# Kernel optimization log

Hardware: AMD Instinct MI355X
Metric: run time of the kernel (lower is better)

The kernel has to match this reference:

```python
import jax, jax.numpy as jnp
import numpy as np
import math

N, S, D, H, L, F = 4, 2048, 512, 8, 4, 200
HD = D // H
EPS = 1e-5


def _pos_encoding(seq_len, d_model, dtype):
    pos = jnp.arange(seq_len, dtype=jnp.float32)[:, None]            # [S,1]
    div = jnp.exp(jnp.arange(0, d_model, 2, dtype=jnp.float32) * (-math.log(10000.0) / d_model))
    ang = pos * div                                                   # [S,D/2]
    pe = jnp.stack([jnp.sin(ang), jnp.cos(ang)], axis=-1).reshape(seq_len, d_model)
    return pe.astype(dtype)


def _layernorm(x, w, b):
    mu = jnp.mean(x, axis=-1, keepdims=True)
    var = jnp.mean(jnp.square(x - mu), axis=-1, keepdims=True)
    return (x - mu) * jax.lax.rsqrt(var + EPS) * w + b


def setup_inputs() -> dict:
    key = jax.random.key(0)
    ks = jax.random.split(key, 8)
    std = 0.02
    inp = {
        "features": jax.random.normal(ks[0], (N, S, D), dtype=jnp.float32),
        # attention projections, stored as [L, in, out] (math-equivalent to torch x @ W.T + b)
        "Wq": jax.random.normal(ks[1], (L, D, D), dtype=jnp.float32) * std,
        "bq": jnp.zeros((L, D), dtype=jnp.float32),
        "Wk": jax.random.normal(ks[2], (L, D, D), dtype=jnp.float32) * std,
        "bk": jnp.zeros((L, D), dtype=jnp.float32),
        "Wv": jax.random.normal(ks[3], (L, D, D), dtype=jnp.float32) * std,
        "bv": jnp.zeros((L, D), dtype=jnp.float32),
        "Wo": jax.random.normal(ks[4], (L, D, D), dtype=jnp.float32) * std,
        "bo": jnp.zeros((L, D), dtype=jnp.float32),
        # FFN
        "W1": jax.random.normal(ks[5], (L, D, F), dtype=jnp.float32) * std,
        "b1": jnp.zeros((L, F), dtype=jnp.float32),
        "W2": jax.random.normal(ks[6], (L, F, D), dtype=jnp.float32) * std,
        "b2": jnp.zeros((L, D), dtype=jnp.float32),
        # layernorms
        "ln1_w": jnp.ones((L, D), dtype=jnp.float32),
        "ln1_b": jnp.zeros((L, D), dtype=jnp.float32),
        "ln2_w": jnp.ones((L, D), dtype=jnp.float32),
        "ln2_b": jnp.zeros((L, D), dtype=jnp.float32),
    }
    return inp


def _encoder(features, Wq, bq, Wk, bk, Wv, bv, Wo, bo, W1, b1, W2, b2,
             ln1_w, ln1_b, ln2_w, ln2_b):
    n, s, d = features.shape
    x = features + _pos_encoding(s, d, features.dtype)[None]  # PositionalEncoding (dropout=identity in eval)
    scale = 1.0 / math.sqrt(HD)
    for l in range(L):
        # MultiHeadAttention: manual QK^T -> softmax -> AV
        q = (x @ Wq[l] + bq[l]).reshape(n, s, H, HD)
        k = (x @ Wk[l] + bk[l]).reshape(n, s, H, HD)
        v = (x @ Wv[l] + bv[l]).reshape(n, s, H, HD)
        attn = jnp.einsum("nshd,nthd->nhst", q, k) * scale          # [N,H,S,S]
        score = jax.nn.softmax(attn, axis=-1)
        y = jnp.einsum("nhst,nthd->nshd", score, v).reshape(n, s, d)
        attn_out = y @ Wo[l] + bo[l]
        x = _layernorm(x + attn_out, ln1_w[l], ln1_b[l])
        # FFN: linear2(relu(linear1(x)))
        ff = jax.nn.relu(x @ W1[l] + b1[l]) @ W2[l] + b2[l]
        x = _layernorm(x + ff, ln2_w[l], ln2_b[l])
    return x


def reference(features, Wq, bq, Wk, bk, Wv, bv, Wo, bo, W1, b1, W2, b2,
              ln1_w, ln1_b, ln2_w, ln2_b):
    return _encoder(features, Wq, bq, Wk, bk, Wv, bv, Wo, bo, W1, b1, W2, b2,
                    ln1_w, ln1_b, ln2_w, ln2_b)
```

## Files before the change

### kernel.cpp

```cpp
#include <hip/hip_runtime.h>
#include <hip/hip_bf16.h>
#include <cstdint>


typedef __bf16 bf16;
typedef __bf16 bf16x8 __attribute__((ext_vector_type(8)));
typedef __bf16 bf16x4 __attribute__((ext_vector_type(4)));
typedef float f32x4 __attribute__((ext_vector_type(4)));

#define MFMA16(a, b, c) __builtin_amdgcn_mfma_f32_16x16x32_bf16((a), (b), (c), 0, 0, 0)

static constexpr int NB   = 4;
static constexpr int SQ   = 2048;
static constexpr int DM   = 512;
static constexpr int NH   = 8;
static constexpr int HD   = 64;
static constexpr int NL   = 4;
static constexpr int FF   = 200;
static constexpr int FFP  = 256;
static constexpr int MTOK = NB * SQ;

__device__ __forceinline__ float fast_exp2(float x) {
#if __has_builtin(__builtin_amdgcn_exp2f)
    return __builtin_amdgcn_exp2f(x);
#else
    return exp2f(x);
#endif
}

__device__ __forceinline__ void gld16(bf16* l, const bf16* g) {
    __builtin_amdgcn_global_load_lds(
        (const __attribute__((address_space(1))) void*)g,
        (__attribute__((address_space(3))) void*)l, 16, 0, 0);
}

__global__ __launch_bounds__(256) void convw_kernel(
    const float* __restrict__ Wq, const float* __restrict__ Wk,
    const float* __restrict__ Wv, const float* __restrict__ Wo,
    const float* __restrict__ W1, const float* __restrict__ W2,
    bf16* __restrict__ wqkvt, bf16* __restrict__ wot,
    bf16* __restrict__ w1t, bf16* __restrict__ w2t)
{
    __shared__ float tile[32][33];
    const int z = blockIdx.z, l = z / 6, which = z % 6;
    const float* src; bf16* dst; int K, Nsrc, Npad, Kpad;
    switch (which) {
        case 0: src = Wq + (size_t)l*DM*DM; dst = wqkvt + (size_t)(l*3+0)*DM*DM; K=DM; Nsrc=DM; Npad=DM; Kpad=DM; break;
        case 1: src = Wk + (size_t)l*DM*DM; dst = wqkvt + (size_t)(l*3+1)*DM*DM; K=DM; Nsrc=DM; Npad=DM; Kpad=DM; break;
        case 2: src = Wv + (size_t)l*DM*DM; dst = wqkvt + (size_t)(l*3+2)*DM*DM; K=DM; Nsrc=DM; Npad=DM; Kpad=DM; break;
        case 3: src = Wo + (size_t)l*DM*DM; dst = wot   + (size_t)l*DM*DM;       K=DM; Nsrc=DM; Npad=DM; Kpad=DM; break;
        case 4: src = W1 + (size_t)l*DM*FF; dst = w1t   + (size_t)l*FFP*DM;      K=DM; Nsrc=FF; Npad=FFP; Kpad=DM; break;
        default:src = W2 + (size_t)l*FF*DM; dst = w2t   + (size_t)l*DM*FFP;      K=FF; Nsrc=DM; Npad=DM; Kpad=FFP; break;
    }
    const int k0 = blockIdx.x * 32, n0 = blockIdx.y * 32;
    if (k0 >= Kpad || n0 >= Npad) return;
    const int tr = threadIdx.x >> 3, tc = (threadIdx.x & 7) * 4;
    for (int c = 0; c < 4; c++) {
        int sr = k0 + tr, sc = n0 + tc + c;
        tile[tr][tc + c] = (sr < K && sc < Nsrc) ? src[(size_t)sr * Nsrc + sc] : 0.f;
    }
    __syncthreads();
    const int dr = n0 + tr;
    if (dr < Npad) {
        for (int c = 0; c < 4; c++) {
            int dc = k0 + tc + c;
            if (dc < Kpad) dst[(size_t)dr * Kpad + dc] = (bf16)tile[tc + c][tr];
        }
    }
}

__global__ __launch_bounds__(256) void posenc_kernel(
    const float* __restrict__ f, float* __restrict__ x, bf16* __restrict__ xb)
{
    const int t = blockIdx.x * 256 + threadIdx.x;
    const int d2 = t & 255, row = t >> 8, s = row & (SQ - 1);
    const float kfac = -0.03597789207803197f;
    float dv = __expf((float)d2 * kfac);
    float ang = (float)s * dv;
    float pe0 = sinf(ang), pe1 = cosf(ang);
    const size_t base = (size_t)row * DM + d2 * 2;
    float2 fv = *(const float2*)(f + base);
    float o0 = fv.x + pe0, o1 = fv.y + pe1;
    *(float2*)(x + base) = make_float2(o0, o1);
    union { bf16 h[2]; unsigned int u; } pk;
    pk.h[0] = (bf16)o0; pk.h[1] = (bf16)o1;
    *(unsigned int*)(xb + base) = pk.u;
}

__device__ __forceinline__ void gemm128_core(
    const bf16* __restrict__ A, const bf16* __restrict__ Wt, int K,
    int m0, int n0, bf16* As, bf16* Bs, f32x4 (&acc)[4][4])
{
    const int tid = threadIdx.x;
    const int w = tid >> 6, lane = tid & 63;
    const int l15 = lane & 15, quad = lane >> 4;
    const int srow = w * 16 + (lane >> 2);
    const int scol = (lane & 3) * 8;
    const bf16* Ag = A  + (size_t)(m0 + srow) * K + scol;
    const bf16* Bg = Wt + (size_t)(n0 + srow) * K + scol;
    bf16* AsW = As + w * 512;
    bf16* BsW = Bs + w * 512;
    const int wm = (w >> 1) * 64, wn = (w & 1) * 64;

    for (int k0 = 0; k0 < K; k0 += 32) {
        __syncthreads();
        gld16(AsW,        Ag + k0);
        gld16(AsW + 2048, Ag + (size_t)64 * K + k0);
        gld16(BsW,        Bg + k0);
        gld16(BsW + 2048, Bg + (size_t)64 * K + k0);
        asm volatile("s_waitcnt vmcnt(0)" ::: "memory");
        __syncthreads();

        bf16x8 af[4], bfr[4];
        #pragma unroll
        for (int i = 0; i < 4; i++)
            af[i] = *(const bf16x8*)&As[(wm + i * 16 + l15) * 32 + quad * 8];
        #pragma unroll
        for (int j = 0; j < 4; j++)
            bfr[j] = *(const bf16x8*)&Bs[(wn + j * 16 + l15) * 32 + quad * 8];
        #pragma unroll
        for (int i = 0; i < 4; i++)
            #pragma unroll
            for (int j = 0; j < 4; j++)
                acc[i][j] = MFMA16(af[i], bfr[j], acc[i][j]);
    }
}

__global__ __launch_bounds__(256, 3) void gemm64_kernel(
    const bf16* __restrict__ A, const bf16* __restrict__ Wt,
    const float* __restrict__ bias, int nbias,
    float* __restrict__ outf, bf16* __restrict__ outb,
    int K, int Nc, int mode)
{
    __shared__ alignas(16) bf16 As[128 * 32];
    __shared__ alignas(16) bf16 Bs[64 * 32];
    const int m0 = blockIdx.x * 128, n0 = blockIdx.y * 64;
    const int tid = threadIdx.x;
    const int w = tid >> 6, lane = tid & 63;
    const int l15 = lane & 15, quad = lane >> 4;
    const int srow = w * 16 + (lane >> 2);
    const int scol = (lane & 3) * 8;
    const bf16* Ag = A  + (size_t)(m0 + srow) * K + scol;
    const bf16* Bg = Wt + (size_t)(n0 + srow) * K + scol;
    bf16* AsW = As + w * 512;
    bf16* BsW = Bs + w * 512;
    const int wm = (w >> 1) * 64, wn = (w & 1) * 32;
    f32x4 acc[4][2] = {};

    for (int k0 = 0; k0 < K; k0 += 32) {
        __syncthreads();
        gld16(AsW,        Ag + k0);
        gld16(AsW + 2048, Ag + (size_t)64 * K + k0);
        gld16(BsW,        Bg + k0);
        asm volatile("s_waitcnt vmcnt(0)" ::: "memory");
        __syncthreads();

        bf16x8 af[4], bfr[2];
        #pragma unroll
        for (int i = 0; i < 4; i++)
            af[i] = *(const bf16x8*)&As[(wm + i * 16 + l15) * 32 + quad * 8];
        #pragma unroll
        for (int j = 0; j < 2; j++)
            bfr[j] = *(const bf16x8*)&Bs[(wn + j * 16 + l15) * 32 + quad * 8];
        #pragma unroll
        for (int i = 0; i < 4; i++)
            #pragma unroll
            for (int j = 0; j < 2; j++)
                acc[i][j] = MFMA16(af[i], bfr[j], acc[i][j]);
    }

    #pragma unroll
    for (int j = 0; j < 2; j++) {
        const int col = n0 + wn + j * 16 + l15;
        const float bv = (col < nbias) ? bias[col] : 0.f;
        #pragma unroll
        for (int i = 0; i < 4; i++) {
            const int rbase = m0 + wm + i * 16 + quad * 4;
            #pragma unroll
            for (int r = 0; r < 4; r++) {
                float v = acc[i][j][r] + bv;
                const int row = rbase + r;
                const size_t idx = (size_t)row * Nc + col;
                if (mode == 0)      outf[idx] = v;
                else if (mode == 1) outb[idx] = (bf16)v;
                else                outb[idx] = (bf16)fmaxf(v, 0.f);
            }
        }
    }
}

__global__ __launch_bounds__(256, 3) void gemm_wo_kernel(
    const bf16* __restrict__ o0, const bf16* __restrict__ o1,
    const float* __restrict__ lpart,
    const bf16* __restrict__ Wt, const float* __restrict__ bias,
    float* __restrict__ outf)
{
    __shared__ alignas(16) bf16 As[128 * 32];
    __shared__ alignas(16) bf16 Bs[64 * 32];
    const int m0 = blockIdx.x * 128, n0 = blockIdx.y * 64;
    const int tid = threadIdx.x;
    const int w = tid >> 6, lane = tid & 63;
    const int l15 = lane & 15, quad = lane >> 4;
    const int srow = w * 16 + (lane >> 2);
    const int scol = (lane & 3) * 8;
    const int row0 = m0 + srow, row1 = row0 + 64;
    const bf16* Bg = Wt + (size_t)(n0 + srow) * DM + scol;
    bf16* BsW = Bs + w * 512;
    bf16* AsD0 = As + w * 512 + lane * 8;
    bf16* AsD1 = AsD0 + 2048;
    const int wm = (w >> 1) * 64, wn = (w & 1) * 32;

    const int b0 = (((row0 >> 11) * 8) << 11) | (row0 & (SQ - 1));
    const int b1 = (((row1 >> 11) * 8) << 11) | (row1 & (SQ - 1));
    float rl0[8], rl1[8];
    #pragma unroll
    for (int h = 0; h < 8; h++) {
        rl0[h] = 1.f / (lpart[b0 + (h << 11)] + lpart[65536 + b0 + (h << 11)]);
        rl1[h] = 1.f / (lpart[b1 + (h << 11)] + lpart[65536 + b1 + (h << 11)]);
    }

    const bf16* A0g  = o0 + (size_t)row0 * DM + scol;
    const bf16* A0g2 = o0 + (size_t)row1 * DM + scol;
    const bf16* A1g  = o1 + (size_t)row0 * DM + scol;
    const bf16* A1g2 = o1 + (size_t)row1 * DM + scol;
    f32x4 acc[4][2] = {};

    #pragma unroll
    for (int h = 0; h < 8; h++) {
        #pragma unroll
        for (int kk = 0; kk < 2; kk++) {
            const int k0 = h * 64 + kk * 32;
            __syncthreads();
            bf16x8 a0 = *(const bf16x8*)(A0g  + k0);
            bf16x8 c0 = *(const bf16x8*)(A1g  + k0);
            bf16x8 a1 = *(const bf16x8*)(A0g2 + k0);
            bf16x8 c1 = *(const bf16x8*)(A1g2 + k0);
            gld16(BsW, Bg + k0);
            bf16x8 s0, s1;
            #pragma unroll
            for (int i = 0; i < 8; i++) {
                s0[i] = (bf16)(((float)a0[i] + (float)c0[i]) * rl0[h]);
                s1[i] = (bf16)(((float)a1[i] + (float)c1[i]) * rl1[h]);
            }
            *(bf16x8*)AsD0 = s0;
            *(bf16x8*)AsD1 = s1;
            asm volatile("s_waitcnt vmcnt(0)" ::: "memory");
            __syncthreads();

            bf16x8 af[4], bfr[2];
            #pragma unroll
            for (int i = 0; i < 4; i++)
                af[i] = *(const bf16x8*)&As[(wm + i * 16 + l15) * 32 + quad * 8];
            #pragma unroll
            for (int j = 0; j < 2; j++)
                bfr[j] = *(const bf16x8*)&Bs[(wn + j * 16 + l15) * 32 + quad * 8];
            #pragma unroll
            for (int i = 0; i < 4; i++)
                #pragma unroll
                for (int j = 0; j < 2; j++)
                    acc[i][j] = MFMA16(af[i], bfr[j], acc[i][j]);
        }
    }

    #pragma unroll
    for (int j = 0; j < 2; j++) {
        const int col = n0 + wn + j * 16 + l15;
        const float bv = bias[col];
        #pragma unroll
        for (int i = 0; i < 4; i++) {
            const int rbase = m0 + wm + i * 16 + quad * 4;
            #pragma unroll
            for (int r = 0; r < 4; r++)
                outf[(size_t)(rbase + r) * DM + col] = acc[i][j][r] + bv;
        }
    }
}

__global__ __launch_bounds__(256, 3) void gemm128_qkv_kernel(
    const bf16* __restrict__ xb, const bf16* __restrict__ Wt,
    const float* __restrict__ bq, const float* __restrict__ bk,
    const float* __restrict__ bv,
    bf16* __restrict__ qb, bf16* __restrict__ kb, bf16* __restrict__ vtb)
{
    __shared__ alignas(16) bf16 As[128 * 32];
    __shared__ alignas(16) bf16 Bs[128 * 32];
    const int m0 = blockIdx.x * 128, n0 = blockIdx.y * 128;
    f32x4 acc[4][4] = {};
    gemm128_core(xb, Wt, DM, m0, n0, As, Bs, acc);

    const int lane = threadIdx.x & 63;
    const int l15 = lane & 15, quad = lane >> 4;
    const int w = threadIdx.x >> 6;
    const int wm = (w >> 1) * 64, wn = (w & 1) * 64;
    const int which = n0 >> 9;
    const float* bias = (which == 0) ? bq : (which == 1) ? bk : bv;
    const float scale = (which == 0) ? 0.18033688f : 1.f;
    #pragma unroll
    for (int j = 0; j < 4; j++) {
        const int c = (n0 & 511) + wn + j * 16 + l15;
        const float bvv = bias[c];
        #pragma unroll
        for (int i = 0; i < 4; i++) {
            const int rbase = m0 + wm + i * 16 + quad * 4;
            #pragma unroll
            for (int r = 0; r < 4; r++) {
                float v = (acc[i][j][r] + bvv) * scale;
                const int row = rbase + r;
                if (which == 0)      qb[(size_t)row * DM + c] = (bf16)v;
                else if (which == 1) kb[(size_t)row * DM + c] = (bf16)v;
                else {
                    const int n = row >> 11, s = row & (SQ - 1);
                    const int h = c >> 6, hd = c & 63;
                    vtb[((size_t)(((n << 3) | h) << 6 | hd) << 11) | s] = (bf16)v;
                }
            }
        }
    }
}

__global__ __launch_bounds__(256, 2) void attn_kernel(
    const bf16* __restrict__ qb, const bf16* __restrict__ kb,
    const bf16* __restrict__ vtb,
    bf16* __restrict__ opart0, bf16* __restrict__ opart1,
    float* __restrict__ lpart)
{
    __shared__ alignas(16) bf16 Kt[2][64][72];
    __shared__ alignas(16) bf16 Vt[2 * 64 * 68];
    const int tid = threadIdx.x;
    const int w = tid >> 6, lane = tid & 63;
    const int l15 = lane & 15, quad = lane >> 4;
    const int id = blockIdx.x;
    const int kvhalf = id & 1;
    const int nh = (id >> 1) & 31;
    const int qblk = id >> 6;
    const int n = nh >> 3, h = nh & 7;
    const int q0 = qblk * 256 + w * 64;
    const int kvbase = kvhalf * (SQ / 2);
    const bf16* qbase = qb + (size_t)n * SQ * DM + h * HD;
    const bf16* kbase = kb + (size_t)n * SQ * DM + h * HD;
    const bf16* vbase = vtb + (size_t)nh * HD * SQ;

    bf16x8 qf[4][2];
    #pragma unroll
    for (int mi = 0; mi < 4; mi++)
        #pragma unroll
        for (int hh = 0; hh < 2; hh++)
            qf[mi][hh] = *(const bf16x8*)(qbase + (size_t)(q0 + mi*16 + l15) * DM + hh*32 + quad*8);

    bf16x8 ones8;
    #pragma unroll
    for (int i = 0; i < 8; i++) ones8[i] = (bf16)1.0f;

    f32x4 o[4][4] = {};
    f32x4 lacc[4] = {};

    const int srow = tid >> 2, seg = (tid & 3) * 16;
    const bf16* krow = kbase + (size_t)(kvbase + srow) * DM + seg;
    const bf16* vrow = vbase + (size_t)srow * SQ + kvbase + seg;

    auto storeV = [&](int buf, bf16x8 a, bf16x8 b) {
        bf16* d = &Vt[(buf * 64 + srow) * 68 + seg];
        bf16x4 p0, p1, p2, p3;
        #pragma unroll
        for (int i = 0; i < 4; i++) { p0[i]=a[i]; p1[i]=a[i+4]; p2[i]=b[i]; p3[i]=b[i+4]; }
        *(bf16x4*)(d)      = p0;
        *(bf16x4*)(d + 4)  = p1;
        *(bf16x4*)(d + 8)  = p2;
        *(bf16x4*)(d + 12) = p3;
    };

    {
        bf16x8 k0 = *(const bf16x8*)(krow);
        bf16x8 k1 = *(const bf16x8*)(krow + 8);
        bf16x8 v0 = *(const bf16x8*)(vrow);
        bf16x8 v1 = *(const bf16x8*)(vrow + 8);
        *(bf16x8*)&Kt[0][srow][seg]     = k0;
        *(bf16x8*)&Kt[0][srow][seg + 8] = k1;
        storeV(0, v0, v1);
    }

    const int NT = SQ / 128;
    for (int jt = 0; jt < NT; jt++) {
        const int buf = jt & 1;
        __syncthreads();
        const bool pre = (jt + 1 < NT);
        bf16x8 k0, k1, v0, v1;
        if (pre) {
            const bf16* kp = krow + (size_t)(jt + 1) * 64 * DM;
            const bf16* vp = vrow + (jt + 1) * 64;
            k0 = *(const bf16x8*)(kp);
            k1 = *(const bf16x8*)(kp + 8);
            v0 = *(const bf16x8*)(vp);
            v1 = *(const bf16x8*)(vp + 8);
        }

        #pragma unroll
        for (int sp = 0; sp < 2; sp++) {
            bf16x8 kfA0 = *(const bf16x8*)&Kt[buf][sp*32 + l15][quad*8];
            bf16x8 kfA1 = *(const bf16x8*)&Kt[buf][sp*32 + l15][32 + quad*8];
            bf16x8 kfB0 = *(const bf16x8*)&Kt[buf][sp*32 + 16 + l15][quad*8];
            bf16x8 kfB1 = *(const bf16x8*)&Kt[buf][sp*32 + 16 + l15][32 + quad*8];
            bf16x8 pf[4];
            #pragma unroll
            for (int mi = 0; mi < 4; mi++) {
                f32x4 sa = {}, sb = {};
                sa = MFMA16(kfA0, qf[mi][0], sa);
                sa = MFMA16(kfA1, qf[mi][1], sa);
                sb = MFMA16(kfB0, qf[mi][0], sb);
                sb = MFMA16(kfB1, qf[mi][1], sb);
                bf16x8 p;
                #pragma unroll
                for (int r = 0; r < 4; r++) {
                    p[r]     = (bf16)fast_exp2(sa[r]);
                    p[r + 4] = (bf16)fast_exp2(sb[r]);
                }
                pf[mi] = p;
                lacc[mi] = MFMA16(p, ones8, lacc[mi]);
            }
            #pragma unroll
            for (int d4 = 0; d4 < 4; d4++) {
                const bf16* vp2 = &Vt[(buf*64 + d4*16 + l15) * 68 + sp*32 + quad*4];
                bf16x4 vlo = *(const bf16x4*)(vp2);
                bf16x4 vhi = *(const bf16x4*)(vp2 + 16);
                bf16x8 vf;
                #pragma unroll
                for (int i = 0; i < 4; i++) { vf[i] = vlo[i]; vf[i+4] = vhi[i]; }
                #pragma unroll
                for (int mi = 0; mi < 4; mi++)
                    o[mi][d4] = MFMA16(pf[mi], vf, o[mi][d4]);
            }
        }

        if (pre) {
            *(bf16x8*)&Kt[buf^1][srow][seg]     = k0;
            *(bf16x8*)&Kt[buf^1][srow][seg + 8] = k1;
            storeV(buf^1, v0, v1);
        }
    }

    if (l15 == 0) {
        const int base = (kvhalf << 16) + (nh << 11) + q0 + quad * 4;
        #pragma unroll
        for (int mi = 0; mi < 4; mi++) {
            float4 v4 = make_float4(lacc[mi][0], lacc[mi][1], lacc[mi][2], lacc[mi][3]);
            *(float4*)&lpart[base + mi * 16] = v4;
        }
    }

    bf16* op = kvhalf ? opart1 : opart0;
    #pragma unroll
    for (int mi = 0; mi < 4; mi++) {
        #pragma unroll
        for (int d4 = 0; d4 < 4; d4++) {
            const int col = h * HD + d4 * 16 + l15;
            #pragma unroll
            for (int r = 0; r < 4; r++) {
                const int row = n * SQ + q0 + mi*16 + quad*4 + r;
                op[(size_t)row * DM + col] = (bf16)o[mi][d4][r];
            }
        }
    }
}

__global__ __launch_bounds__(256) void ln_kernel(
    const float* __restrict__ res, const float* __restrict__ add,
    const float* __restrict__ g, const float* __restrict__ beta,
    float* __restrict__ outf, bf16* __restrict__ outb)
{
    const int w = threadIdx.x >> 6, lane = threadIdx.x & 63;
    const size_t row = (size_t)blockIdx.x * 4 + w;
    const float4* rp = (const float4*)(res + row * DM);
    const float4* ap = (const float4*)(add + row * DM);
    float4 v[2];
    float s = 0.f, s2 = 0.f;
    #pragma unroll
    for (int i = 0; i < 2; i++) {
        const int idx = i * 64 + lane;
        float4 a = rp[idx], c = ap[idx];
        float x0 = a.x + c.x, x1 = a.y + c.y, x2 = a.z + c.z, x3 = a.w + c.w;
        v[i] = make_float4(x0, x1, x2, x3);
        s  += x0 + x1 + x2 + x3;
        s2 += x0*x0 + x1*x1 + x2*x2 + x3*x3;
    }
    for (int m = 1; m < 64; m <<= 1) {
        s  += __shfl_xor(s,  m, 64);
        s2 += __shfl_xor(s2, m, 64);
    }
    const float mean = s * (1.f / DM);
    const float var  = s2 * (1.f / DM) - mean * mean;
    const float rstd = rsqrtf(var + 1e-5f);
    #pragma unroll
    for (int i = 0; i < 2; i++) {
        const int idx = i * 64 + lane;
        float4 gw = ((const float4*)g)[idx], bw = ((const float4*)beta)[idx];
        float o0 = (v[i].x - mean) * rstd * gw.x + bw.x;
        float o1 = (v[i].y - mean) * rstd * gw.y + bw.y;
        float o2 = (v[i].z - mean) * rstd * gw.z + bw.z;
        float o3 = (v[i].w - mean) * rstd * gw.w + bw.w;
        ((float4*)(outf + row * DM))[idx] = make_float4(o0, o1, o2, o3);
        union { bf16 h[4]; uint2 u; } pk;
        pk.h[0] = (bf16)o0; pk.h[1] = (bf16)o1; pk.h[2] = (bf16)o2; pk.h[3] = (bf16)o3;
        *(uint2*)(outb + row * DM + idx * 4) = pk.u;
    }
}

extern "C" void kernel_launch(void* const* d_in, const int* in_sizes, int n_in,
                              void* d_out, int out_size, void* d_ws, size_t ws_size,
                              hipStream_t stream)
{
    const float* features = (const float*)d_in[0];
    const float* Wq  = (const float*)d_in[1];
    const float* bq  = (const float*)d_in[2];
    const float* Wk  = (const float*)d_in[3];
    const float* bk  = (const float*)d_in[4];
    const float* Wv  = (const float*)d_in[5];
    const float* bv  = (const float*)d_in[6];
    const float* Wo  = (const float*)d_in[7];
    const float* bo  = (const float*)d_in[8];
    const float* W1  = (const float*)d_in[9];
    const float* b1  = (const float*)d_in[10];
    const float* W2  = (const float*)d_in[11];
    const float* b2  = (const float*)d_in[12];
    const float* ln1w = (const float*)d_in[13];
    const float* ln1b = (const float*)d_in[14];
    const float* ln2w = (const float*)d_in[15];
    const float* ln2b = (const float*)d_in[16];
    float* outp = (float*)d_out;

    char* p = (char*)d_ws;
    size_t off = 0;
    auto alloc = [&](size_t bytes) { void* r = p + off; off = (off + bytes + 255) & ~(size_t)255; return r; };
    const size_t tokD = (size_t)MTOK * DM;
    float* x     = (float*)alloc(tokD * 4);
    float* tmp   = (float*)alloc(tokD * 4);
    bf16* xb     = (bf16*)alloc(tokD * 2);
    bf16* qb     = (bf16*)alloc(tokD * 2);
    bf16* kb     = (bf16*)alloc(tokD * 2);
    bf16* vtb    = (bf16*)alloc(tokD * 2);
    bf16* opart0 = (bf16*)alloc(tokD * 2);
    bf16* opart1 = (bf16*)alloc(tokD * 2);
    float* lpart = (float*)alloc(2 * 65536 * 4);
    bf16* ffh    = (bf16*)alloc((size_t)MTOK * FFP * 2);
    bf16* wqkvt  = (bf16*)alloc((size_t)NL * 3 * DM * DM * 2);
    bf16* wot    = (bf16*)alloc((size_t)NL * DM * DM * 2);
    bf16* w1t    = (bf16*)alloc((size_t)NL * FFP * DM * 2);
    bf16* w2t    = (bf16*)alloc((size_t)NL * DM * FFP * 2);
    (void)ws_size; (void)in_sizes; (void)n_in; (void)out_size;

    convw_kernel<<<dim3(16, 16, NL * 6), 256, 0, stream>>>(
        Wq, Wk, Wv, Wo, W1, W2, wqkvt, wot, w1t, w2t);

    posenc_kernel<<<MTOK, 256, 0, stream>>>(features, x, xb);

    for (int l = 0; l < NL; l++) {
        const bf16* wqkvt_l = wqkvt + (size_t)l * 3 * DM * DM;
        gemm128_qkv_kernel<<<dim3(MTOK / 128, 1536 / 128), 256, 0, stream>>>(
            xb, wqkvt_l, bq + l*DM, bk + l*DM, bv + l*DM, qb, kb, vtb);
        attn_kernel<<<512, 256, 0, stream>>>(qb, kb, vtb, opart0, opart1, lpart);
        gemm_wo_kernel<<<dim3(MTOK / 128, DM / 64), 256, 0, stream>>>(
            opart0, opart1, lpart, wot + (size_t)l*DM*DM, bo + l*DM, tmp);
        ln_kernel<<<MTOK / 4, 256, 0, stream>>>(x, tmp, ln1w + l*DM, ln1b + l*DM, x, xb);
        gemm64_kernel<<<dim3(MTOK / 128, FFP / 64), 256, 0, stream>>>(
            xb, w1t + (size_t)l*FFP*DM, b1 + l*FF, FF, nullptr, ffh, DM, FFP, 2);
        gemm64_kernel<<<dim3(MTOK / 128, DM / 64), 256, 0, stream>>>(
            ffh, w2t + (size_t)l*DM*FFP, b2 + l*DM, DM, tmp, nullptr, FFP, DM, 0);
        float* outdst = (l == NL - 1) ? outp : x;
        ln_kernel<<<MTOK / 4, 256, 0, stream>>>(x, tmp, ln2w + l*DM, ln2b + l*DM, outdst, xb);
    }
}
```

Before: 624.9 us.

## Double-buffer LDS tiles in GEMM kernels to overlap global loads with MFMA

```diff
diff --git a/kernel.cpp b/kernel.cpp
--- a/kernel.cpp
+++ b/kernel.cpp
@@ -32,6 +32,11 @@
     __builtin_amdgcn_global_load_lds(
         (const __attribute__((address_space(1))) void*)g,
         (__attribute__((address_space(3))) void*)l, 16, 0, 0);
+}
+
+__device__ __forceinline__ void drain_and_barrier() {
+    asm volatile("s_waitcnt vmcnt(0) lgkmcnt(0)" ::: "memory");
+    __builtin_amdgcn_s_barrier();
 }
 
 __global__ __launch_bounds__(256) void convw_kernel(
@@ -98,42 +103,51 @@
     const int scol = (lane & 3) * 8;
     const bf16* Ag = A  + (size_t)(m0 + srow) * K + scol;
     const bf16* Bg = Wt + (size_t)(n0 + srow) * K + scol;
-    bf16* AsW = As + w * 512;
-    bf16* BsW = Bs + w * 512;
     const int wm = (w >> 1) * 64, wn = (w & 1) * 64;
 
-    for (int k0 = 0; k0 < K; k0 += 32) {
-        __syncthreads();
+    auto stage = [&](int buf, int k0) {
+        bf16* AsW = As + buf * 4096 + w * 512;
+        bf16* BsW = Bs + buf * 4096 + w * 512;
         gld16(AsW,        Ag + k0);
         gld16(AsW + 2048, Ag + (size_t)64 * K + k0);
         gld16(BsW,        Bg + k0);
         gld16(BsW + 2048, Bg + (size_t)64 * K + k0);
-        asm volatile("s_waitcnt vmcnt(0)" ::: "memory");
-        __syncthreads();
-
+    };
+
+    stage(0, 0);
+    drain_and_barrier();
+
+    const int nsteps = K >> 5;
+    int buf = 0;
+    for (int t = 0; t < nsteps; ++t) {
+        if (t + 1 < nsteps) stage(buf ^ 1, (t + 1) << 5);
+        const bf16* AsR = As + buf * 4096;
+        const bf16* BsR = Bs + buf * 4096;
         bf16x8 af[4], bfr[4];
         #pragma unroll
         for (int i = 0; i < 4; i++)
-            af[i] = *(const bf16x8*)&As[(wm + i * 16 + l15) * 32 + quad * 8];
+            af[i] = *(const bf16x8*)&AsR[(wm + i * 16 + l15) * 32 + quad * 8];
         #pragma unroll
         for (int j = 0; j < 4; j++)
-            bfr[j] = *(const bf16x8*)&Bs[(wn + j * 16 + l15) * 32 + quad * 8];
+            bfr[j] = *(const bf16x8*)&BsR[(wn + j * 16 + l15) * 32 + quad * 8];
         #pragma unroll
         for (int i = 0; i < 4; i++)
             #pragma unroll
             for (int j = 0; j < 4; j++)
                 acc[i][j] = MFMA16(af[i], bfr[j], acc[i][j]);
-    }
-}
-
-__global__ __launch_bounds__(256, 3) void gemm64_kernel(
+        drain_and_barrier();
+        buf ^= 1;
+    }
+}
+
+__global__ __launch_bounds__(256, 4) void gemm64_kernel(
     const bf16* __restrict__ A, const bf16* __restrict__ Wt,
     const float* __restrict__ bias, int nbias,
     float* __restrict__ outf, bf16* __restrict__ outb,
     int K, int Nc, int mode)
 {
-    __shared__ alignas(16) bf16 As[128 * 32];
-    __shared__ alignas(16) bf16 Bs[64 * 32];
+    __shared__ alignas(16) bf16 As[2 * 128 * 32];
+    __shared__ alignas(16) bf16 Bs[2 * 64 * 32];
     const int m0 = blockIdx.x * 128, n0 = blockIdx.y * 64;
     const int tid = threadIdx.x;
     const int w = tid >> 6, lane = tid & 63;
@@ -142,31 +156,40 @@
     const int scol = (lane & 3) * 8;
     const bf16* Ag = A  + (size_t)(m0 + srow) * K + scol;
     const bf16* Bg = Wt + (size_t)(n0 + srow) * K + scol;
-    bf16* AsW = As + w * 512;
-    bf16* BsW = Bs + w * 512;
     const int wm = (w >> 1) * 64, wn = (w & 1) * 32;
     f32x4 acc[4][2] = {};
 
-    for (int k0 = 0; k0 < K; k0 += 32) {
-        __syncthreads();
+    auto stage = [&](int buf, int k0) {
+        bf16* AsW = As + buf * 4096 + w * 512;
+        bf16* BsW = Bs + buf * 2048 + w * 512;
         gld16(AsW,        Ag + k0);
         gld16(AsW + 2048, Ag + (size_t)64 * K + k0);
         gld16(BsW,        Bg + k0);
-        asm volatile("s_waitcnt vmcnt(0)" ::: "memory");
-        __syncthreads();
-
+    };
+
+    stage(0, 0);
+    drain_and_barrier();
+
+    const int nsteps = K >> 5;
+    int buf = 0;
+    for (int t = 0; t < nsteps; ++t) {
+        if (t + 1 < nsteps) stage(buf ^ 1, (t + 1) << 5);
+        const bf16* AsR = As + buf * 4096;
+        const bf16* BsR = Bs + buf * 2048;
         bf16x8 af[4], bfr[2];
         #pragma unroll
         for (int i = 0; i < 4; i++)
-            af[i] = *(const bf16x8*)&As[(wm + i * 16 + l15) * 32 + quad * 8];
+            af[i] = *(const bf16x8*)&AsR[(wm + i * 16 + l15) * 32 + quad * 8];
         #pragma unroll
         for (int j = 0; j < 2; j++)
-            bfr[j] = *(const bf16x8*)&Bs[(wn + j * 16 + l15) * 32 + quad * 8];
+            bfr[j] = *(const bf16x8*)&BsR[(wn + j * 16 + l15) * 32 + quad * 8];
         #pragma unroll
         for (int i = 0; i < 4; i++)
             #pragma unroll
             for (int j = 0; j < 2; j++)
                 acc[i][j] = MFMA16(af[i], bfr[j], acc[i][j]);
+        drain_and_barrier();
+        buf ^= 1;
     }
 
     #pragma unroll
@@ -189,14 +212,14 @@
     }
 }
 
-__global__ __launch_bounds__(256, 3) void gemm_wo_kernel(
+__global__ __launch_bounds__(256, 4) void gemm_wo_kernel(
     const bf16* __restrict__ o0, const bf16* __restrict__ o1,
     const float* __restrict__ lpart,
     const bf16* __restrict__ Wt, const float* __restrict__ bias,
     float* __restrict__ outf)
 {
-    __shared__ alignas(16) bf16 As[128 * 32];
-    __shared__ alignas(16) bf16 Bs[64 * 32];
+    __shared__ alignas(16) bf16 As[2 * 128 * 32];
+    __shared__ alignas(16) bf16 Bs[2 * 64 * 32];
     const int m0 = blockIdx.x * 128, n0 = blockIdx.y * 64;
     const int tid = threadIdx.x;
     const int w = tid >> 6, lane = tid & 63;
@@ -205,9 +228,6 @@
     const int scol = (lane & 3) * 8;
     const int row0 = m0 + srow, row1 = row0 + 64;
     const bf16* Bg = Wt + (size_t)(n0 + srow) * DM + scol;
-    bf16* BsW = Bs + w * 512;
-    bf16* AsD0 = As + w * 512 + lane * 8;
-    bf16* AsD1 = AsD0 + 2048;
     const int wm = (w >> 1) * 64, wn = (w & 1) * 32;
 
     const int b0 = (((row0 >> 11) * 8) << 11) | (row0 & (SQ - 1));
@@ -225,41 +245,59 @@
     const bf16* A1g2 = o1 + (size_t)row1 * DM + scol;
     f32x4 acc[4][2] = {};
 
-    #pragma unroll
-    for (int h = 0; h < 8; h++) {
-        #pragma unroll
-        for (int kk = 0; kk < 2; kk++) {
-            const int k0 = h * 64 + kk * 32;
-            __syncthreads();
-            bf16x8 a0 = *(const bf16x8*)(A0g  + k0);
-            bf16x8 c0 = *(const bf16x8*)(A1g  + k0);
-            bf16x8 a1 = *(const bf16x8*)(A0g2 + k0);
-            bf16x8 c1 = *(const bf16x8*)(A1g2 + k0);
-            gld16(BsW, Bg + k0);
-            bf16x8 s0, s1;
-            #pragma unroll
-            for (int i = 0; i < 8; i++) {
-                s0[i] = (bf16)(((float)a0[i] + (float)c0[i]) * rl0[h]);
-                s1[i] = (bf16)(((float)a1[i] + (float)c1[i]) * rl1[h]);
-            }
-            *(bf16x8*)AsD0 = s0;
-            *(bf16x8*)AsD1 = s1;
-            asm volatile("s_waitcnt vmcnt(0)" ::: "memory");
-            __syncthreads();
-
-            bf16x8 af[4], bfr[2];
-            #pragma unroll
-            for (int i = 0; i < 4; i++)
-                af[i] = *(const bf16x8*)&As[(wm + i * 16 + l15) * 32 + quad * 8];
+    auto combineStore = [&](int buf, int h, bf16x8 a0, bf16x8 c0, bf16x8 a1, bf16x8 c1) {
+        bf16x8 s0, s1;
+        #pragma unroll
+        for (int i = 0; i < 8; i++) {
+            s0[i] = (bf16)(((float)a0[i] + (float)c0[i]) * rl0[h]);
+            s1[i] = (bf16)(((float)a1[i] + (float)c1[i]) * rl1[h]);
+        }
+        bf16* d = As + buf * 4096 + w * 512 + lane * 8;
+        *(bf16x8*)d          = s0;
+        *(bf16x8*)(d + 2048) = s1;
+    };
+
+    {
+        bf16x8 a0 = *(const bf16x8*)(A0g);
+        bf16x8 c0 = *(const bf16x8*)(A1g);
+        bf16x8 a1 = *(const bf16x8*)(A0g2);
+        bf16x8 c1 = *(const bf16x8*)(A1g2);
+        gld16(Bs + w * 512, Bg);
+        combineStore(0, 0, a0, c0, a1, c1);
+        drain_and_barrier();
+    }
+
+    int buf = 0;
+    for (int t = 0; t < 16; ++t) {
+        const bool pre = (t + 1 < 16);
+        bf16x8 na0, nc0, na1, nc1;
+        if (pre) {
+            const int k1 = (t + 1) * 32;
+            na0 = *(const bf16x8*)(A0g  + k1);
+            nc0 = *(const bf16x8*)(A1g  + k1);
+            na1 = *(const bf16x8*)(A0g2 + k1);
+            nc1 = *(const bf16x8*)(A1g2 + k1);
+            gld16(Bs + (buf ^ 1) * 2048 + w * 512, Bg + k1);
+        }
+
+        const bf16* AsR = As + buf * 4096;
+        const bf16* BsR = Bs + buf * 2048;
+        bf16x8 af[4], bfr[2];
+        #pragma unroll
+        for (int i = 0; i < 4; i++)
+            af[i] = *(const bf16x8*)&AsR[(wm + i * 16 + l15) * 32 + quad * 8];
+        #pragma unroll
+        for (int j = 0; j < 2; j++)
+            bfr[j] = *(const bf16x8*)&BsR[(wn + j * 16 + l15) * 32 + quad * 8];
+        #pragma unroll
+        for (int i = 0; i < 4; i++)
             #pragma unroll
             for (int j = 0; j < 2; j++)
-                bfr[j] = *(const bf16x8*)&Bs[(wn + j * 16 + l15) * 32 + quad * 8];
-            #pragma unroll
-            for (int i = 0; i < 4; i++)
-                #pragma unroll
-                for (int j = 0; j < 2; j++)
-                    acc[i][j] = MFMA16(af[i], bfr[j], acc[i][j]);
-        }
+                acc[i][j] = MFMA16(af[i], bfr[j], acc[i][j]);
+
+        if (pre) combineStore(buf ^ 1, (t + 1) >> 1, na0, nc0, na1, nc1);
+        drain_and_barrier();
+        buf ^= 1;
     }
 
     #pragma unroll
@@ -276,14 +314,14 @@
     }
 }
 
-__global__ __launch_bounds__(256, 3) void gemm128_qkv_kernel(
+__global__ __launch_bounds__(256, 4) void gemm128_qkv_kernel(
     const bf16* __restrict__ xb, const bf16* __restrict__ Wt,
     const float* __restrict__ bq, const float* __restrict__ bk,
     const float* __restrict__ bv,
     bf16* __restrict__ qb, bf16* __restrict__ kb, bf16* __restrict__ vtb)
 {
-    __shared__ alignas(16) bf16 As[128 * 32];
-    __shared__ alignas(16) bf16 Bs[128 * 32];
+    __shared__ alignas(16) bf16 As[2 * 128 * 32];
+    __shared__ alignas(16) bf16 Bs[2 * 128 * 32];
     const int m0 = blockIdx.x * 128, n0 = blockIdx.y * 128;
     f32x4 acc[4][4] = {};
     gemm128_core(xb, Wt, DM, m0, n0, As, Bs, acc);
```

Result: no change. 618.6 us (-1.0%).
